# Kernel optimization log

Hardware: AMD Instinct MI355X
Metric: run time of the kernel (lower is better)

## Reference

```python
import jax, jax.numpy as jnp
import numpy as np

N, E, HID, H, L, R = 20000, 160000, 512, 8, 4, 128
DK = HID // H
SCALE = 1.0 / np.sqrt(DK)
EPS = 1e-5


def setup_inputs() -> dict:
    key = jax.random.key(0)
    ks = jax.random.split(key, 24)
    p = lambda i, shape: jax.random.normal(ks[i], shape, jnp.float32) * 0.02
    return {
        'x': jax.random.normal(ks[0], (N, HID), jnp.float32),
        'relations': jax.random.randint(ks[1], (E,), 0, R),
        'src': jax.random.randint(ks[2], (E,), 0, N),
        'dst': jax.random.randint(ks[3], (E,), 0, N),
        'rel_embed': p(4, (R, HID)),
        'Wq': p(5, (L, HID, HID)), 'bq': jnp.zeros((L, HID), jnp.float32),
        'Wk': p(6, (L, HID, HID)), 'bk': jnp.zeros((L, HID), jnp.float32),
        'Wv': p(7, (L, HID, HID)), 'bv': jnp.zeros((L, HID), jnp.float32),
        'Wo': p(8, (L, HID, HID)), 'bo': jnp.zeros((L, HID), jnp.float32),
        'W1': p(9, (L, HID, 4 * HID)), 'b1': jnp.zeros((L, 4 * HID), jnp.float32),
        'W2': p(10, (L, 4 * HID, HID)), 'b2': jnp.zeros((L, HID), jnp.float32),
        'ln1_g': jnp.ones((L, HID), jnp.float32), 'ln1_b': jnp.zeros((L, HID), jnp.float32),
        'ln2_g': jnp.ones((L, HID), jnp.float32), 'ln2_b': jnp.zeros((L, HID), jnp.float32),
    }


def _ln(x, g, b):
    m = x.mean(-1, keepdims=True)
    v = jnp.square(x - m).mean(-1, keepdims=True)
    return (x - m) * jax.lax.rsqrt(v + EPS) * g + b


def _layer(x, rh, src, dst, Wq, bq, Wk, bk, Wv, bv, Wo, bo, W1, b1, W2, b2, g1, bb1, g2, bb2):
    # rh: (E, H, DK) per-edge relation features
    q = (x @ Wq + bq).reshape(N, H, DK)
    k = (x @ Wk + bk).reshape(N, H, DK)
    v = (x @ Wv + bv).reshape(N, H, DK)
    # edge score: ((k_src + r) . q_dst) / sqrt(d_k)   -> (E, H)
    score = jnp.einsum('ehd,ehd->eh', k[src] + rh, q[dst]) * SCALE
    # segment softmax over incoming edges of each dst node
    smax = jax.ops.segment_max(score, dst, num_segments=N)
    smax = jnp.where(jnp.isfinite(smax), smax, 0.0)  # nodes with no in-edges
    ex = jnp.exp(score - smax[dst])                   # (E, H)
    z = jax.ops.segment_sum(ex, dst, num_segments=N)  # (N, H)
    wv = jax.ops.segment_sum(ex[:, :, None] * (v[src] + rh), dst, num_segments=N)  # (N, H, DK)
    o = wv / (z[:, :, None] + 1e-9)
    o = o.reshape(N, HID) @ Wo + bo
    h = _ln(x + o, g1, bb1)
    ff = jax.nn.relu(h @ W1 + b1) @ W2 + b2
    return _ln(h + ff, g2, bb2)


def reference(x, relations, src, dst, rel_embed, Wq, bq, Wk, bk, Wv, bv, Wo, bo, W1, b1, W2, b2, ln1_g, ln1_b, ln2_g, ln2_b):
    lg_x = rel_embed[relations]            # (E, HID), shared across layers
    rh = lg_x.reshape(E, H, DK)
    for i in range(L):
        x = _layer(x, rh, src, dst, Wq[i], bq[i], Wk[i], bk[i], Wv[i], bv[i],
                   Wo[i], bo[i], W1[i], b1[i], W2[i], b2[i],
                   ln1_g[i], ln1_b[i], ln2_g[i], ln2_b[i])
    return x
```

## Files before the change

kernel.cpp:

```cpp
#include <hip/hip_runtime.h>
#include <cstdint>
#include <cstddef>

#define N_NODES 20000
#define N_EDGES 160000
#define HIDDEN  512
#define NHEAD   8
#define HDK     64
#define NLAYER  4
#define FFDIM   2048
#define ATT_SCALE 0.125f
#define S1C 262144
#define S2C 1048576
#define WLYR (4 * S1C + 2 * S2C)

typedef float  f4  __attribute__((ext_vector_type(4)));
typedef short  s8v __attribute__((ext_vector_type(8)));
typedef __bf16 b8v __attribute__((ext_vector_type(8)));

template <typename V>
__device__ inline auto mfma_try(V a, V b, f4 c, int)
    -> decltype(__builtin_amdgcn_mfma_f32_16x16x32_bf16(a, b, c, 0, 0, 0)) {
  return __builtin_amdgcn_mfma_f32_16x16x32_bf16(a, b, c, 0, 0, 0);
}
template <typename V>
__device__ inline f4 mfma_try(V a, V b, f4 c, long) {
  return __builtin_amdgcn_mfma_f32_16x16x32_bf16(
      __builtin_bit_cast(b8v, a), __builtin_bit_cast(b8v, b), c, 0, 0, 0);
}
__device__ inline f4 mfma_bf16(s8v a, s8v b, f4 c) { return mfma_try(a, b, c, 0); }

__device__ __forceinline__ unsigned short f2bf(float f) {
  unsigned u = __builtin_bit_cast(unsigned, f);
  u += 0x7FFFu + ((u >> 16) & 1u);
  return (unsigned short)(u >> 16);
}
__device__ __forceinline__ float bf2f(unsigned short u) {
  return __builtin_bit_cast(float, (unsigned)u << 16);
}

#define GLOAD_LDS16(gp, lp)                                                   \
  __builtin_amdgcn_global_load_lds(                                           \
      (const __attribute__((address_space(1))) void*)(gp),                    \
      (__attribute__((address_space(3))) void*)(lp), 16, 0, 0)

__global__ void cast_kernel(const float* __restrict__ in, unsigned short* __restrict__ out, int n) {
  int i = blockIdx.x * blockDim.x + threadIdx.x;
  if (i < n) out[i] = f2bf(in[i]);
}

__global__ void weight_prep_kernel(const float* __restrict__ Wq, const float* __restrict__ Wk,
                                   const float* __restrict__ Wv, const float* __restrict__ Wo_,
                                   const float* __restrict__ W1, const float* __restrict__ W2,
                                   const float* __restrict__ bq, const float* __restrict__ bk,
                                   const float* __restrict__ bv,
                                   unsigned short* __restrict__ wAll, float* __restrict__ bqkvAll) {
  int l = blockIdx.x / 3078;
  int id = blockIdx.x % 3078;
  unsigned short* wqkv = wAll + (size_t)l * WLYR;
  unsigned short* wo = wqkv + 3 * S1C;
  unsigned short* w1 = wo + S1C;
  unsigned short* w2 = w1 + S2C;
  if (id >= 3072) {
    int i = (id - 3072) * 256 + threadIdx.y * 32 + threadIdx.x;
    float* bqkv = bqkvAll + l * 1536;
    if (i < 512) bqkv[i] = bq[l * 512 + i];
    else if (i < 1024) bqkv[i] = bk[l * 512 + i - 512];
    else if (i < 1536) bqkv[i] = bv[l * 512 + i - 1024];
    return;
  }
  const float* in; unsigned short* out; int K, N, bx, by;
  if (id < 1024) {
    int m = id >> 8, t = id & 255;
    in = ((m == 0) ? Wq : (m == 1) ? Wk : (m == 2) ? Wv : Wo_) + (size_t)l * S1C;
    out = (m == 3) ? wo : wqkv + m * S1C;
    K = 512; N = 512; bx = t & 15; by = t >> 4;
  } else if (id < 2048) {
    int t = id - 1024;
    in = W1 + (size_t)l * S2C; out = w1; K = 512; N = 2048; bx = t & 63; by = t >> 6;
  } else {
    int t = id - 2048;
    in = W2 + (size_t)l * S2C; out = w2; K = 2048; N = 512; bx = t & 15; by = t >> 4;
  }
  __shared__ float t32[32][33];
  int tx = threadIdx.x, ty = threadIdx.y;
  int n0 = bx * 32, k0 = by * 32;
  int Kc = K >> 3;
#pragma unroll
  for (int i = 0; i < 32; i += 8)
    t32[ty + i][tx] = in[(size_t)(k0 + ty + i) * N + n0 + tx];
  __syncthreads();
#pragma unroll
  for (int i = 0; i < 32; i += 8) {
    int n = n0 + ty + i, k = k0 + tx;
    size_t idx = ((size_t)(n >> 4) * Kc + (k >> 3)) * 128 + (n & 15) * 8 + (k & 7);
    out[idx] = f2bf(t32[tx][ty + i]);
  }
}

#define BM 128
#define BN 128
#define BK 64

template <bool OBF16>
__global__ __launch_bounds__(256, 3) void gemm_bf16(
    const unsigned short* __restrict__ A, const unsigned short* __restrict__ Bt,
    const float* __restrict__ bias, void* __restrict__ Cp,
    int M, int K, int N, int relu) {
  __shared__ __align__(16) unsigned short As[8192];
  int tid = threadIdx.x;
  int wave = tid >> 6, lane = tid & 63;
  int quad = lane >> 4, l16 = lane & 15;
  int wm = (wave >> 1) * 64, wn = (wave & 1) * 64;

  int T = gridDim.x * gridDim.y;
  int i = blockIdx.y * gridDim.x + blockIdx.x;
  int C = T >> 3;
  int w = (i < (C << 3)) ? ((i & 7) * C + (i >> 3)) : i;
  int bx = w % gridDim.x, by = w / gridDim.x;
  int m0 = by * BM, n0 = bx * BN;

  f4 acc[4][4];
#pragma unroll
  for (int i2 = 0; i2 < 4; ++i2)
#pragma unroll
    for (int j = 0; j < 4; ++j) acc[i2][j] = (f4){0.f, 0.f, 0.f, 0.f};

  int rbase = wave * 8 + (lane >> 3);
  int q8 = (lane & 7) ^ ((lane >> 3) & 7);
  const unsigned short* aptr[4];
#pragma unroll
  for (int j = 0; j < 4; ++j) {
    int r = j * 32 + rbase;
    int gm = m0 + r; if (gm >= M) gm = M - 1;
    aptr[j] = A + (size_t)gm * K + q8 * 8;
  }

  int Kc = K >> 3;
  const unsigned short* bbase = Bt + quad * 128 + l16 * 8;
  size_t nioff[4];
#pragma unroll
  for (int i2 = 0; i2 < 4; ++i2)
    nioff[i2] = ((size_t)((n0 >> 4) + (wn >> 4) + i2) * Kc) * 128;

  int nk = K >> 6;
  for (int ks = 0; ks < nk; ++ks) {
#pragma unroll
    for (int j = 0; j < 4; ++j)
      GLOAD_LDS16(aptr[j], &As[j * 2048 + wave * 512]);
    s8v bfr[2][4];
#pragma unroll
    for (int s = 0; s < 2; ++s)
#pragma unroll
      for (int i2 = 0; i2 < 4; ++i2)
        bfr[s][i2] = *(const s8v*)(bbase + nioff[i2] + (size_t)ks * 1024 + s * 512);
#pragma unroll
    for (int j = 0; j < 4; ++j) aptr[j] += BK;
    __syncthreads();
#pragma unroll
    for (int s = 0; s < 2; ++s) {
      s8v af[4];
#pragma unroll
      for (int i2 = 0; i2 < 4; ++i2) {
        int ra = wm + i2 * 16 + l16;
        af[i2] = *(const s8v*)(&As[ra * 64 + ((((s << 2) | quad) ^ (ra & 7)) * 8)]);
      }
#pragma unroll
      for (int mi = 0; mi < 4; ++mi)
#pragma unroll
        for (int ni = 0; ni < 4; ++ni)
          acc[mi][ni] = mfma_bf16(af[mi], bfr[s][ni], acc[mi][ni]);
    }
    __syncthreads();
  }

  if constexpr (OBF16) {
    unsigned short* Cs = As + wave * 1088;
    float bvv[4];
#pragma unroll
    for (int ni = 0; ni < 4; ++ni) bvv[ni] = bias[n0 + wn + ni * 16 + l16];
    int row_l = lane >> 2, cg = lane & 3;
#pragma unroll
    for (int mi = 0; mi < 4; ++mi) {
#pragma unroll
      for (int ni = 0; ni < 4; ++ni) {
#pragma unroll
        for (int r = 0; r < 4; ++r) {
          float val = acc[mi][ni][r] + bvv[ni];
          if (relu) val = fmaxf(val, 0.f);
          Cs[(quad * 4 + r) * 68 + ni * 16 + l16] = f2bf(val);
        }
      }
      s8v v0 = *(const s8v*)(&Cs[row_l * 68 + cg * 16]);
      s8v v1 = *(const s8v*)(&Cs[row_l * 68 + cg * 16 + 8]);
      int grow = m0 + wm + mi * 16 + row_l;
      if (grow < M) {
        unsigned short* cp = (unsigned short*)Cp + (size_t)grow * N + n0 + wn + cg * 16;
        *(s8v*)cp = v0;
        *(s8v*)(cp + 8) = v1;
      }
    }
  } else {
#pragma unroll
    for (int ni = 0; ni < 4; ++ni) {
      int col = n0 + wn + ni * 16 + l16;
      float bv = bias[col];
#pragma unroll
      for (int mi = 0; mi < 4; ++mi) {
#pragma unroll
        for (int r = 0; r < 4; ++r) {
          int row = m0 + wm + mi * 16 + quad * 4 + r;
          if (row < M) {
            float val = acc[mi][ni][r] + bv;
            if (relu) val = fmaxf(val, 0.f);
            ((float*)Cp)[(size_t)row * N + col] = val;
          }
        }
      }
    }
  }
}

__global__ void hist_kernel(const int* __restrict__ dst, int* __restrict__ cnt, int E) {
  int e = blockIdx.x * blockDim.x + threadIdx.x;
  if (e < E) atomicAdd(&cnt[dst[e]], 1);
}

__global__ void scan_kernel(const int* __restrict__ cnt, int* __restrict__ offs, int n) {
  __shared__ int sh[1024];
  __shared__ int carry_sh;
  int tid = threadIdx.x;
  if (tid == 0) carry_sh = 0;
  __syncthreads();
  for (int base = 0; base < n; base += 1024) {
    int v = (base + tid < n) ? cnt[base + tid] : 0;
    sh[tid] = v;
    __syncthreads();
    for (int s = 1; s < 1024; s <<= 1) {
      int t = (tid >= s) ? sh[tid - s] : 0;
      __syncthreads();
      sh[tid] += t;
      __syncthreads();
    }
    int carry = carry_sh;
    if (base + tid < n) offs[base + tid] = carry + sh[tid] - v;
    __syncthreads();
    if (tid == 1023) carry_sh = carry + sh[1023];
    __syncthreads();
  }
  if (tid == 0) offs[n] = carry_sh;
}

__global__ void scatter_kernel(const int* __restrict__ dst, const int* __restrict__ src,
                               const int* __restrict__ relations, const int* __restrict__ offs,
                               int* __restrict__ cursor, int* __restrict__ esrc,
                               int* __restrict__ erel, int E) {
  int e = blockIdx.x * blockDim.x + threadIdx.x;
  if (e < E) {
    int d = dst[e];
    int pos = offs[d] + atomicAdd(&cursor[d], 1);
    esrc[pos] = src[e];
    erel[pos] = relations[e];
  }
}

__global__ void edge_attn_kernel(const unsigned short* __restrict__ q,
                                 const unsigned short* __restrict__ k,
                                 const unsigned short* __restrict__ v,
                                 const unsigned short* __restrict__ relb,
                                 const int* __restrict__ offs,
                                 const int* __restrict__ esrc,
                                 const int* __restrict__ erel,
                                 unsigned short* __restrict__ o, int Nn, int STR) {
  int wid = (blockIdx.x * blockDim.x + threadIdx.x) >> 6;
  int lane = threadIdx.x & 63;
  if (wid >= Nn) return;
  int base = (lane >> 3) * HDK + (lane & 7) * 8;

  s8v qv = *(const s8v*)(q + (size_t)wid * STR + base);
  float qf[8];
#pragma unroll
  for (int j = 0; j < 8; ++j) qf[j] = bf2f((unsigned short)qv[j]);

  int beg = offs[wid], end = offs[wid + 1];
  float m = -1e30f, z = 0.f;
  float acc[8];
#pragma unroll
  for (int j = 0; j < 8; ++j) acc[j] = 0.f;

  s8v kv = {}, vv = {}, rv = {};
  if (beg < end) {
    int s0 = esrc[beg], r0 = erel[beg];
    kv = *(const s8v*)(k + (size_t)s0 * STR + base);
    vv = *(const s8v*)(v + (size_t)s0 * STR + base);
    rv = *(const s8v*)(relb + (size_t)r0 * HIDDEN + base);
  }
  for (int i = beg; i < end; ++i) {
    s8v kc = kv, vc = vv, rc = rv;
    if (i + 1 < end) {
      int sn = esrc[i + 1], rn = erel[i + 1];
      kv = *(const s8v*)(k + (size_t)sn * STR + base);
      vv = *(const s8v*)(v + (size_t)sn * STR + base);
      rv = *(const s8v*)(relb + (size_t)rn * HIDDEN + base);
    }
    float rf[8], p = 0.f;
#pragma unroll
    for (int j = 0; j < 8; ++j) {
      rf[j] = bf2f((unsigned short)rc[j]);
      p += (bf2f((unsigned short)kc[j]) + rf[j]) * qf[j];
    }
    p += __shfl_xor(p, 1, 64);
    p += __shfl_xor(p, 2, 64);
    p += __shfl_xor(p, 4, 64);
    p *= ATT_SCALE;
    float mn = fmaxf(m, p);
    float a = __expf(m - mn);
    float wgt = __expf(p - mn);
    z = z * a + wgt;
#pragma unroll
    for (int j = 0; j < 8; ++j)
      acc[j] = acc[j] * a + wgt * (bf2f((unsigned short)vc[j]) + rf[j]);
    m = mn;
  }
  float rz = 1.f / (z + 1e-9f);
  s8v ov;
#pragma unroll
  for (int j = 0; j < 8; ++j) ov[j] = (short)f2bf(acc[j] * rz);
  *(s8v*)(o + (size_t)wid * HIDDEN + base) = ov;
}

template <bool WF32>
__global__ void ln_kernel(const unsigned short* __restrict__ xp, const unsigned short* __restrict__ y,
                          const float* __restrict__ g, const float* __restrict__ b,
                          float* __restrict__ outf, unsigned short* __restrict__ outb, int Nn) {
  int wid = (blockIdx.x * blockDim.x + threadIdx.x) >> 6;
  int lane = threadIdx.x & 63;
  if (wid >= Nn) return;
  int base = lane * 8;
  s8v xv = *(const s8v*)(xp + (size_t)wid * HIDDEN + base);
  s8v yv = *(const s8v*)(y + (size_t)wid * HIDDEN + base);
  float vals[8];
  float sum = 0.f;
#pragma unroll
  for (int j = 0; j < 8; ++j) {
    vals[j] = bf2f((unsigned short)xv[j]) + bf2f((unsigned short)yv[j]);
    sum += vals[j];
  }
#pragma unroll
  for (int off = 32; off; off >>= 1) sum += __shfl_xor(sum, off, 64);
  float mean = sum * (1.f / 512.f);
  float sq = 0.f;
#pragma unroll
  for (int j = 0; j < 8; ++j) { float d = vals[j] - mean; sq += d * d; }
#pragma unroll
  for (int off = 32; off; off >>= 1) sq += __shfl_xor(sq, off, 64);
  float rstd = rsqrtf(sq * (1.f / 512.f) + 1e-5f);
  f4 gv0 = *(const f4*)(g + base);
  f4 gv1 = *(const f4*)(g + base + 4);
  f4 bv0 = *(const f4*)(b + base);
  f4 bv1 = *(const f4*)(b + base + 4);
  float ov_f[8];
#pragma unroll
  for (int j = 0; j < 4; ++j) {
    ov_f[j]     = (vals[j]     - mean) * rstd * gv0[j] + bv0[j];
    ov_f[j + 4] = (vals[j + 4] - mean) * rstd * gv1[j] + bv1[j];
  }
  s8v ov;
#pragma unroll
  for (int j = 0; j < 8; ++j) ov[j] = (short)f2bf(ov_f[j]);
  *(s8v*)(outb + (size_t)wid * HIDDEN + base) = ov;
  if constexpr (WF32) {
    f4 o0, o1;
#pragma unroll
    for (int j = 0; j < 4; ++j) { o0[j] = ov_f[j]; o1[j] = ov_f[j + 4]; }
    *(f4*)(outf + (size_t)wid * HIDDEN + base) = o0;
    *(f4*)(outf + (size_t)wid * HIDDEN + base + 4) = o1;
  }
}

extern "C" void kernel_launch(void* const* d_in, const int* in_sizes, int n_in,
                              void* d_out, int out_size, void* d_ws, size_t ws_size,
                              hipStream_t stream) {
  const float* x0        = (const float*)d_in[0];
  const int*   relations = (const int*)d_in[1];
  const int*   src       = (const int*)d_in[2];
  const int*   dst       = (const int*)d_in[3];
  const float* rel_embed = (const float*)d_in[4];
  const float* Wq = (const float*)d_in[5];  const float* bq = (const float*)d_in[6];
  const float* Wk = (const float*)d_in[7];  const float* bk = (const float*)d_in[8];
  const float* Wv = (const float*)d_in[9];  const float* bv = (const float*)d_in[10];
  const float* Wo = (const float*)d_in[11]; const float* bo = (const float*)d_in[12];
  const float* W1 = (const float*)d_in[13]; const float* b1 = (const float*)d_in[14];
  const float* W2 = (const float*)d_in[15]; const float* b2 = (const float*)d_in[16];
  const float* g1  = (const float*)d_in[17]; const float* bb1 = (const float*)d_in[18];
  const float* g2  = (const float*)d_in[19]; const float* bb2 = (const float*)d_in[20];
  float* xout = (float*)d_out;

  const size_t S1 = S1C;
  const size_t S2 = S2C;
  const size_t NH = (size_t)N_NODES * HIDDEN;

  unsigned short* wAll = (unsigned short*)d_ws;
  float* bqkvAll = (float*)(wAll + (size_t)NLAYER * WLYR);
  unsigned short* arena = (unsigned short*)(bqkvAll + NLAYER * 1536);
  unsigned short* qkvb = arena;
  unsigned short* ob   = arena + 3 * NH;
  unsigned short* ff1  = arena;
  unsigned short* proj = arena;
  unsigned short* hbb = arena + 4 * NH;
  unsigned short* xb  = hbb + NH;
  unsigned short* projb = xb + NH;
  unsigned short* relb  = projb + NH;
  int* cnt    = (int*)(relb + 65536);
  int* offs   = cnt + N_NODES;
  int* cursor = offs + N_NODES + 1;
  int* esrc   = cursor + N_NODES;
  int* erel   = esrc + N_EDGES;

  hipMemsetAsync(cnt, 0, N_NODES * sizeof(int), stream);
  hipMemsetAsync(cursor, 0, N_NODES * sizeof(int), stream);
  hist_kernel<<<(N_EDGES + 255) / 256, 256, 0, stream>>>(dst, cnt, N_EDGES);
  scan_kernel<<<1, 1024, 0, stream>>>(cnt, offs, N_NODES);
  scatter_kernel<<<(N_EDGES + 255) / 256, 256, 0, stream>>>(dst, src, relations, offs, cursor, esrc, erel, N_EDGES);
  cast_kernel<<<(int)((NH + 255) / 256), 256, 0, stream>>>(x0, xb, (int)NH);
  cast_kernel<<<256, 256, 0, stream>>>(rel_embed, relb, 65536);
  dim3 tb(32, 8);
  weight_prep_kernel<<<NLAYER * 3078, tb, 0, stream>>>(Wq, Wk, Wv, Wo, W1, W2, bq, bk, bv,
                                                       wAll, bqkvAll);

  const int MBc = (N_NODES + BM - 1) / BM;

  for (int l = 0; l < NLAYER; ++l) {
    unsigned short* wqkv = wAll + (size_t)l * WLYR;
    unsigned short* wo = wqkv + 3 * S1;
    unsigned short* w1 = wo + S1;
    unsigned short* w2 = w1 + S2;
    float* bqkv = bqkvAll + l * 1536;
    gemm_bf16<true><<<dim3(12, MBc), 256, 0, stream>>>(xb, wqkv, bqkv, qkvb, N_NODES, 512, 1536, 0);
    edge_attn_kernel<<<(N_NODES + 3) / 4, 256, 0, stream>>>(qkvb, qkvb + 512, qkvb + 1024,
                                                            relb, offs, esrc, erel, ob, N_NODES, 1536);
    gemm_bf16<true><<<dim3(4, MBc), 256, 0, stream>>>(ob, wo, bo + l * 512, proj, N_NODES, 512, 512, 0);
    ln_kernel<false><<<N_NODES / 4, 256, 0, stream>>>(xb, proj, g1 + l * 512, bb1 + l * 512, nullptr, hbb, N_NODES);
    gemm_bf16<true><<<dim3(16, MBc), 256, 0, stream>>>(hbb, w1, b1 + l * 2048, ff1, N_NODES, 512, 2048, 1);
    gemm_bf16<true><<<dim3(4, MBc), 256, 0, stream>>>(ff1, w2, b2 + l * 512, projb, N_NODES, 2048, 512, 0);
    if (l == NLAYER - 1)
      ln_kernel<true><<<N_NODES / 4, 256, 0, stream>>>(hbb, projb, g2 + l * 512, bb2 + l * 512, xout, xb, N_NODES);
    else
      ln_kernel<false><<<N_NODES / 4, 256, 0, stream>>>(hbb, projb, g2 + l * 512, bb2 + l * 512, nullptr, xb, N_NODES);
  }
}
```

Baseline: 1.217 ms.

## Add 256x256-tile pipelined bf16 GEMM for QKV and FFN1 projections

Adds a new 512-thread GEMM kernel that uses 256x256 output tiles, double-buffered LDS staging via global_load_lds, and an XCD-aware block remap. MFMA work is interleaved with the next tile's loads, under explicit barriers and priority hints. Epilogue stores go through LDS for vectorized bf16 writes. It replaces the existing GEMM for the QKV and W1 projections to raise data reuse and overlap loads with compute, at the cost of 128KB dynamic LDS per block and lower occupancy.

```diff
diff --git a/kernel.cpp b/kernel.cpp
--- a/kernel.cpp
+++ b/kernel.cpp
@@ -43,6 +43,12 @@
   __builtin_amdgcn_global_load_lds(                                           \
       (const __attribute__((address_space(1))) void*)(gp),                    \
       (__attribute__((address_space(3))) void*)(lp), 16, 0, 0)
+
+__device__ __forceinline__ void wg_barrier() {
+  asm volatile("" ::: "memory");
+  __builtin_amdgcn_s_barrier();
+  asm volatile("" ::: "memory");
+}
 
 __global__ void cast_kernel(const float* __restrict__ in, unsigned short* __restrict__ out, int n) {
   int i = blockIdx.x * blockDim.x + threadIdx.x;
@@ -221,6 +227,146 @@
   }
 }
 
+__global__ __launch_bounds__(512, 2) void gemm256(
+    const unsigned short* __restrict__ A, const unsigned short* __restrict__ Bt,
+    const float* __restrict__ bias, unsigned short* __restrict__ Cp,
+    int M, int K, int N, int relu) {
+  extern __shared__ __align__(16) unsigned short smem[];
+  int tid = threadIdx.x;
+  int wave = tid >> 6, lane = tid & 63;
+  int quad = lane >> 4, l16 = lane & 15;
+  int wr = wave >> 2, wc = wave & 3;
+  int wr2 = wr * 128, wc4 = wc * 4;
+
+  int T = gridDim.x * gridDim.y;
+  int orig = blockIdx.y * gridDim.x + blockIdx.x;
+  int sq = T >> 3, sr = T & 7;
+  int xcd = orig & 7, loc = orig >> 3;
+  int w = (xcd < sr ? xcd * (sq + 1) : sr * (sq + 1) + (xcd - sr) * sq) + loc;
+  int bx = w % gridDim.x, by = w / gridDim.x;
+  int m0 = by * 256, n0 = bx * 256;
+
+  f4 acc[8][4];
+#pragma unroll
+  for (int i2 = 0; i2 < 8; ++i2)
+#pragma unroll
+    for (int j = 0; j < 4; ++j) acc[i2][j] = (f4){0.f, 0.f, 0.f, 0.f};
+
+  int rbase = wave * 8 + (lane >> 3);
+  int q8 = (lane & 7) ^ ((lane >> 3) & 7);
+  const unsigned short* aptr[4];
+#pragma unroll
+  for (int j = 0; j < 4; ++j) {
+    int gm = m0 + j * 64 + rbase; if (gm >= M) gm = M - 1;
+    aptr[j] = A + (size_t)gm * K + q8 * 8;
+  }
+  int Kc = K >> 3;
+  const unsigned short* bptr[2][2];
+#pragma unroll
+  for (int s = 0; s < 2; ++s)
+#pragma unroll
+    for (int j = 0; j < 2; ++j)
+      bptr[s][j] = Bt + (((size_t)(n0 >> 4) + wave * 2 + j) * Kc + s * 4) * 128 + lane * 8;
+
+#define STAGE_A256(c, h, ko) \
+  GLOAD_LDS16(aptr[2*(h)]   + (ko), &smem[(c)*32768 + ((2*(h))*64   + wave*8)*64 + lane*8]); \
+  GLOAD_LDS16(aptr[2*(h)+1] + (ko), &smem[(c)*32768 + ((2*(h)+1)*64 + wave*8)*64 + lane*8]);
+#define STAGE_B256(c, s, ko) \
+  GLOAD_LDS16(bptr[s][0] + (ko), &smem[(c)*32768 + 16384 + ((s)*16 + wave*2    )*512 + lane*8]); \
+  GLOAD_LDS16(bptr[s][1] + (ko), &smem[(c)*32768 + 16384 + ((s)*16 + wave*2 + 1)*512 + lane*8]);
+#define AFRAGS(c, mh, s) \
+  _Pragma("unroll") for (int i2 = 0; i2 < 4; ++i2) { \
+    int ra = wr2 + ((mh)*4 + i2) * 16 + l16; \
+    af[i2] = *(const s8v*)(&smem[(c)*32768 + ra*64 + ((((s)*4 + quad) ^ (l16 & 7)) * 8)]); \
+  }
+#define BFRAGS(c, s) \
+  _Pragma("unroll") for (int ni = 0; ni < 4; ++ni) \
+    bf[ni] = *(const s8v*)(&smem[(c)*32768 + 16384 + ((s)*16 + wc4 + ni) * 512 + lane * 8]);
+#define ENDPH() \
+  wg_barrier(); \
+  asm volatile("s_waitcnt lgkmcnt(0)" ::: "memory"); \
+  __builtin_amdgcn_sched_barrier(0);
+#define MFMA16(mh) \
+  __builtin_amdgcn_s_setprio(1); \
+  _Pragma("unroll") for (int mi = 0; mi < 4; ++mi) \
+    _Pragma("unroll") for (int ni = 0; ni < 4; ++ni) \
+      acc[(mh)*4 + mi][ni] = mfma_bf16(af[mi], bf[ni], acc[(mh)*4 + mi][ni]); \
+  __builtin_amdgcn_s_setprio(0);
+
+  s8v af[4], bf[4];
+  int nt = K >> 6;
+  STAGE_A256(0, 0, 0); STAGE_A256(0, 1, 0); STAGE_B256(0, 0, 0); STAGE_B256(0, 1, 0);
+  asm volatile("s_waitcnt vmcnt(2)" ::: "memory");
+  wg_barrier();
+
+  for (int t = 0; t < nt - 1; ++t) {
+    const int c = t & 1, d = c ^ 1;
+    const int ka = (t + 1) * 64, kb = (t + 1) * 1024;
+    {
+      AFRAGS(c, 0, 0); BFRAGS(c, 0);
+      STAGE_A256(d, 0, ka);
+      ENDPH(); MFMA16(0); wg_barrier();
+    }
+    {
+      AFRAGS(c, 1, 0);
+      STAGE_A256(d, 1, ka);
+      asm volatile("s_waitcnt vmcnt(4)" ::: "memory");
+      ENDPH(); MFMA16(1); wg_barrier();
+    }
+    {
+      AFRAGS(c, 0, 1); BFRAGS(c, 1);
+      STAGE_B256(d, 0, kb);
+      ENDPH(); MFMA16(0); wg_barrier();
+    }
+    {
+      AFRAGS(c, 1, 1);
+      STAGE_B256(d, 1, kb);
+      asm volatile("s_waitcnt vmcnt(2)" ::: "memory");
+      ENDPH(); MFMA16(1); wg_barrier();
+    }
+  }
+  {
+    const int c = (nt - 1) & 1;
+    { AFRAGS(c, 0, 0); BFRAGS(c, 0); ENDPH(); MFMA16(0); wg_barrier(); }
+    { AFRAGS(c, 1, 0);
+      asm volatile("s_waitcnt vmcnt(0)" ::: "memory");
+      ENDPH(); MFMA16(1); wg_barrier(); }
+    { AFRAGS(c, 0, 1); BFRAGS(c, 1); ENDPH(); MFMA16(0); wg_barrier(); }
+    { AFRAGS(c, 1, 1); ENDPH(); MFMA16(1); wg_barrier(); }
+  }
+
+  unsigned short* Cs = smem + wave * 1088;
+  float bvv[4];
+#pragma unroll
+  for (int ni = 0; ni < 4; ++ni) bvv[ni] = bias[n0 + wc * 64 + ni * 16 + l16];
+  int row_l = lane >> 2, cg = lane & 3;
+#pragma unroll
+  for (int mi = 0; mi < 8; ++mi) {
+#pragma unroll
+    for (int ni = 0; ni < 4; ++ni)
+#pragma unroll
+      for (int r = 0; r < 4; ++r) {
+        float val = acc[mi][ni][r] + bvv[ni];
+        if (relu) val = fmaxf(val, 0.f);
+        Cs[(quad * 4 + r) * 68 + ni * 16 + l16] = f2bf(val);
+      }
+    s8v v0 = *(const s8v*)(&Cs[row_l * 68 + cg * 16]);
+    s8v v1 = *(const s8v*)(&Cs[row_l * 68 + cg * 16 + 8]);
+    int grow = m0 + wr2 + mi * 16 + row_l;
+    if (grow < M) {
+      unsigned short* cp = Cp + (size_t)grow * N + n0 + wc * 64 + cg * 16;
+      *(s8v*)cp = v0;
+      *(s8v*)(cp + 8) = v1;
+    }
+  }
+#undef STAGE_A256
+#undef STAGE_B256
+#undef AFRAGS
+#undef BFRAGS
+#undef ENDPH
+#undef MFMA16
+}
+
 __global__ void hist_kernel(const int* __restrict__ dst, int* __restrict__ cnt, int E) {
   int e = blockIdx.x * blockDim.x + threadIdx.x;
   if (e < E) atomicAdd(&cnt[dst[e]], 1);
@@ -417,6 +563,8 @@
   int* esrc   = cursor + N_NODES;
   int* erel   = esrc + N_EDGES;
 
+  hipFuncSetAttribute((const void*)gemm256, hipFuncAttributeMaxDynamicSharedMemorySize, 131072);
+
   hipMemsetAsync(cnt, 0, N_NODES * sizeof(int), stream);
   hipMemsetAsync(cursor, 0, N_NODES * sizeof(int), stream);
   hist_kernel<<<(N_EDGES + 255) / 256, 256, 0, stream>>>(dst, cnt, N_EDGES);
@@ -429,6 +577,7 @@
                                                        wAll, bqkvAll);
 
   const int MBc = (N_NODES + BM - 1) / BM;
+  const int MB2 = (N_NODES + 255) / 256;
 
   for (int l = 0; l < NLAYER; ++l) {
     unsigned short* wqkv = wAll + (size_t)l * WLYR;
@@ -436,12 +585,12 @@
     unsigned short* w1 = wo + S1;
     unsigned short* w2 = w1 + S2;
     float* bqkv = bqkvAll + l * 1536;
-    gemm_bf16<true><<<dim3(12, MBc), 256, 0, stream>>>(xb, wqkv, bqkv, qkvb, N_NODES, 512, 1536, 0);
+    gemm256<<<dim3(6, MB2), 512, 131072, stream>>>(xb, wqkv, bqkv, qkvb, N_NODES, 512, 1536, 0);
     edge_attn_kernel<<<(N_NODES + 3) / 4, 256, 0, stream>>>(qkvb, qkvb + 512, qkvb + 1024,
                                                             relb, offs, esrc, erel, ob, N_NODES, 1536);
     gemm_bf16<true><<<dim3(4, MBc), 256, 0, stream>>>(ob, wo, bo + l * 512, proj, N_NODES, 512, 512, 0);
     ln_kernel<false><<<N_NODES / 4, 256, 0, stream>>>(xb, proj, g1 + l * 512, bb1 + l * 512, nullptr, hbb, N_NODES);
-    gemm_bf16<true><<<dim3(16, MBc), 256, 0, stream>>>(hbb, w1, b1 + l * 2048, ff1, N_NODES, 512, 2048, 1);
+    gemm256<<<dim3(8, MB2), 512, 131072, stream>>>(hbb, w1, b1 + l * 2048, ff1, N_NODES, 512, 2048, 1);
     gemm_bf16<true><<<dim3(4, MBc), 256, 0, stream>>>(ff1, w2, b2 + l * 512, projb, N_NODES, 2048, 512, 0);
     if (l == NLAYER - 1)
       ln_kernel<true><<<N_NODES / 4, 256, 0, stream>>>(hbb, projb, g2 + l * 512, bb2 + l * 512, xout, xb, N_NODES);
```

New measurement: 1.283 ms. +5.4%, slower.

## Double-buffer A tiles in LDS and prefetch B fragments in bf16 GEMM

Applied to the files above, without the earlier changes.

The GEMM main loop now uses two LDS buffers for the A tile and two register sets for the B fragments. The next K-step's global-to-LDS load and B register loads are issued before computing the current step, which is meant to hide memory latency behind the MFMAs. This doubles LDS use (32KB per block) and adds B registers, which may lower occupancy under launch_bounds(256,3). The loop is unrolled by two and assumes nk is even, which holds for K of 512 and 2048.

```diff
diff --git a/kernel.cpp b/kernel.cpp
--- a/kernel.cpp
+++ b/kernel.cpp
@@ -107,7 +107,7 @@
     const unsigned short* __restrict__ A, const unsigned short* __restrict__ Bt,
     const float* __restrict__ bias, void* __restrict__ Cp,
     int M, int K, int N, int relu) {
-  __shared__ __align__(16) unsigned short As[8192];
+  __shared__ __align__(16) unsigned short As[2][8192];
   int tid = threadIdx.x;
   int wave = tid >> 6, lane = tid & 63;
   int quad = lane >> 4, l16 = lane & 15;
@@ -143,39 +143,48 @@
   for (int i2 = 0; i2 < 4; ++i2)
     nioff[i2] = ((size_t)((n0 >> 4) + (wn >> 4) + i2) * Kc) * 128;
 
+#define STAGE_A(buf, koff)                                                    \
+  _Pragma("unroll") for (int j = 0; j < 4; ++j)                               \
+    GLOAD_LDS16(aptr[j] + (koff), &As[buf][j * 2048 + wave * 512]);
+#define LOAD_B(dst, t)                                                        \
+  _Pragma("unroll") for (int s = 0; s < 2; ++s)                               \
+    _Pragma("unroll") for (int i2 = 0; i2 < 4; ++i2)                          \
+      dst[s][i2] = *(const s8v*)(bbase + nioff[i2] + (size_t)(t) * 1024 + s * 512);
+#define COMPUTE(buf, bset)                                                    \
+  _Pragma("unroll") for (int s = 0; s < 2; ++s) {                             \
+    s8v af[4];                                                                \
+    _Pragma("unroll") for (int i2 = 0; i2 < 4; ++i2) {                        \
+      int ra = wm + i2 * 16 + l16;                                            \
+      af[i2] = *(const s8v*)(&As[buf][ra * 64 + ((((s << 2) | quad) ^ (ra & 7)) * 8)]); \
+    }                                                                         \
+    _Pragma("unroll") for (int mi = 0; mi < 4; ++mi)                          \
+      _Pragma("unroll") for (int ni = 0; ni < 4; ++ni)                        \
+        acc[mi][ni] = mfma_bf16(af[mi], bset[s][ni], acc[mi][ni]);            \
+  }
+
+  s8v b0[2][4], b1[2][4];
   int nk = K >> 6;
-  for (int ks = 0; ks < nk; ++ks) {
-#pragma unroll
-    for (int j = 0; j < 4; ++j)
-      GLOAD_LDS16(aptr[j], &As[j * 2048 + wave * 512]);
-    s8v bfr[2][4];
-#pragma unroll
-    for (int s = 0; s < 2; ++s)
-#pragma unroll
-      for (int i2 = 0; i2 < 4; ++i2)
-        bfr[s][i2] = *(const s8v*)(bbase + nioff[i2] + (size_t)ks * 1024 + s * 512);
-#pragma unroll
-    for (int j = 0; j < 4; ++j) aptr[j] += BK;
+  STAGE_A(0, 0);
+  LOAD_B(b0, 0);
+  __syncthreads();
+  for (int t = 0; t < nk; t += 2) {
+    STAGE_A(1, (t + 1) * 64);
+    LOAD_B(b1, t + 1);
+    COMPUTE(0, b0);
     __syncthreads();
-#pragma unroll
-    for (int s = 0; s < 2; ++s) {
-      s8v af[4];
-#pragma unroll
-      for (int i2 = 0; i2 < 4; ++i2) {
-        int ra = wm + i2 * 16 + l16;
-        af[i2] = *(const s8v*)(&As[ra * 64 + ((((s << 2) | quad) ^ (ra & 7)) * 8)]);
-      }
-#pragma unroll
-      for (int mi = 0; mi < 4; ++mi)
-#pragma unroll
-        for (int ni = 0; ni < 4; ++ni)
-          acc[mi][ni] = mfma_bf16(af[mi], bfr[s][ni], acc[mi][ni]);
-    }
+    if (t + 2 < nk) {
+      STAGE_A(0, (t + 2) * 64);
+      LOAD_B(b0, t + 2);
+    }
+    COMPUTE(1, b1);
     __syncthreads();
   }
+#undef STAGE_A
+#undef LOAD_B
+#undef COMPUTE
 
   if constexpr (OBF16) {
-    unsigned short* Cs = As + wave * 1088;
+    unsigned short* Cs = &As[0][0] + wave * 1088;
     float bvv[4];
 #pragma unroll
     for (int ni = 0; ni < 4; ++ni) bvv[ni] = bias[n0 + wn + ni * 16 + l16];
```

Result: no change. 1.220 ms (+0.2%).

## Parallelize CSR offset scan across blocks and deepen edge gather prefetch to two

Applied to the files above, without the earlier changes.

The serial single-block prefix scan over node in-degree counts is replaced by a three-kernel scan: per-block inclusive scans, a tiny serial pass over the block sums, and a fix-up that writes the offsets. The goal is to remove a long serial chain of barriers from setup. Separately, the edge attention kernel now prefetches the k, v and relation vectors two edges ahead instead of one, which hides more gather latency at the cost of extra registers. Two extra kernel launches and scratch buffers are added.

```diff
diff --git a/kernel.cpp b/kernel.cpp
--- a/kernel.cpp
+++ b/kernel.cpp
@@ -226,29 +226,37 @@
   if (e < E) atomicAdd(&cnt[dst[e]], 1);
 }
 
-__global__ void scan_kernel(const int* __restrict__ cnt, int* __restrict__ offs, int n) {
+__global__ void scan_blk_kernel(const int* __restrict__ cnt, int* __restrict__ incl,
+                                int* __restrict__ bsum, int n) {
   __shared__ int sh[1024];
-  __shared__ int carry_sh;
   int tid = threadIdx.x;
-  if (tid == 0) carry_sh = 0;
+  int gi = blockIdx.x * 1024 + tid;
+  int v = (gi < n) ? cnt[gi] : 0;
+  sh[tid] = v;
   __syncthreads();
-  for (int base = 0; base < n; base += 1024) {
-    int v = (base + tid < n) ? cnt[base + tid] : 0;
-    sh[tid] = v;
+  for (int s = 1; s < 1024; s <<= 1) {
+    int t = (tid >= s) ? sh[tid - s] : 0;
     __syncthreads();
-    for (int s = 1; s < 1024; s <<= 1) {
-      int t = (tid >= s) ? sh[tid - s] : 0;
-      __syncthreads();
-      sh[tid] += t;
-      __syncthreads();
-    }
-    int carry = carry_sh;
-    if (base + tid < n) offs[base + tid] = carry + sh[tid] - v;
+    sh[tid] += t;
     __syncthreads();
-    if (tid == 1023) carry_sh = carry + sh[1023];
-    __syncthreads();
-  }
-  if (tid == 0) offs[n] = carry_sh;
+  }
+  if (gi < n) incl[gi] = sh[tid];
+  if (tid == 1023) bsum[blockIdx.x] = sh[1023];
+}
+
+__global__ void scan_mid_kernel(const int* __restrict__ bsum, int* __restrict__ boff, int nb) {
+  if (threadIdx.x == 0 && blockIdx.x == 0) {
+    int run = 0;
+    for (int i = 0; i < nb; ++i) { boff[i] = run; run += bsum[i]; }
+    boff[nb] = run;
+  }
+}
+
+__global__ void scan_fix_kernel(const int* __restrict__ incl, const int* __restrict__ boff,
+                                int* __restrict__ offs, int n) {
+  int gi = blockIdx.x * 1024 + threadIdx.x;
+  if (gi < n) offs[gi + 1] = boff[blockIdx.x] + incl[gi];
+  if (gi == 0) offs[0] = 0;
 }
 
 __global__ void scatter_kernel(const int* __restrict__ dst, const int* __restrict__ src,
@@ -288,20 +296,28 @@
 #pragma unroll
   for (int j = 0; j < 8; ++j) acc[j] = 0.f;
 
-  s8v kv = {}, vv = {}, rv = {};
+  s8v kvA = {}, vvA = {}, rvA = {};
+  s8v kvB = {}, vvB = {}, rvB = {};
   if (beg < end) {
     int s0 = esrc[beg], r0 = erel[beg];
-    kv = *(const s8v*)(k + (size_t)s0 * STR + base);
-    vv = *(const s8v*)(v + (size_t)s0 * STR + base);
-    rv = *(const s8v*)(relb + (size_t)r0 * HIDDEN + base);
+    kvA = *(const s8v*)(k + (size_t)s0 * STR + base);
+    vvA = *(const s8v*)(v + (size_t)s0 * STR + base);
+    rvA = *(const s8v*)(relb + (size_t)r0 * HIDDEN + base);
+  }
+  if (beg + 1 < end) {
+    int s1 = esrc[beg + 1], r1 = erel[beg + 1];
+    kvB = *(const s8v*)(k + (size_t)s1 * STR + base);
+    vvB = *(const s8v*)(v + (size_t)s1 * STR + base);
+    rvB = *(const s8v*)(relb + (size_t)r1 * HIDDEN + base);
   }
   for (int i = beg; i < end; ++i) {
-    s8v kc = kv, vc = vv, rc = rv;
-    if (i + 1 < end) {
-      int sn = esrc[i + 1], rn = erel[i + 1];
-      kv = *(const s8v*)(k + (size_t)sn * STR + base);
-      vv = *(const s8v*)(v + (size_t)sn * STR + base);
-      rv = *(const s8v*)(relb + (size_t)rn * HIDDEN + base);
+    s8v kc = kvA, vc = vvA, rc = rvA;
+    kvA = kvB; vvA = vvB; rvA = rvB;
+    if (i + 2 < end) {
+      int sn = esrc[i + 2], rn = erel[i + 2];
+      kvB = *(const s8v*)(k + (size_t)sn * STR + base);
+      vvB = *(const s8v*)(v + (size_t)sn * STR + base);
+      rvB = *(const s8v*)(relb + (size_t)rn * HIDDEN + base);
     }
     float rf[8], p = 0.f;
 #pragma unroll
@@ -416,11 +432,17 @@
   int* cursor = offs + N_NODES + 1;
   int* esrc   = cursor + N_NODES;
   int* erel   = esrc + N_EDGES;
+  int* sincl  = erel + N_EDGES;
+  int* sbsum  = sincl + 20480;
+  int* sboff  = sbsum + 32;
 
   hipMemsetAsync(cnt, 0, N_NODES * sizeof(int), stream);
   hipMemsetAsync(cursor, 0, N_NODES * sizeof(int), stream);
   hist_kernel<<<(N_EDGES + 255) / 256, 256, 0, stream>>>(dst, cnt, N_EDGES);
-  scan_kernel<<<1, 1024, 0, stream>>>(cnt, offs, N_NODES);
+  const int NB = (N_NODES + 1023) / 1024;
+  scan_blk_kernel<<<NB, 1024, 0, stream>>>(cnt, sincl, sbsum, N_NODES);
+  scan_mid_kernel<<<1, 64, 0, stream>>>(sbsum, sboff, NB);
+  scan_fix_kernel<<<NB, 1024, 0, stream>>>(sincl, sboff, offs, N_NODES);
   scatter_kernel<<<(N_EDGES + 255) / 256, 256, 0, stream>>>(dst, src, relations, offs, cursor, esrc, erel, N_EDGES);
   cast_kernel<<<(int)((NH + 255) / 256), 256, 0, stream>>>(x0, xb, (int)NH);
   cast_kernel<<<256, 256, 0, stream>>>(rel_embed, relb, 65536);
```

Measured after the change: 1.192 ms. -2.1%, faster.
